# Optimization experiments

Hardware: AMD Instinct MI355X
Metric: run time of the kernel (lower is better)

## Reference

```python
import jax, jax.numpy as jnp
import numpy as np

B, T, C = 2, 2048, 2048
N_HEAD, N_GROUPS, HEAD_SIZE = 16, 4, 128
Q_PER_KV = N_HEAD // N_GROUPS


def setup_inputs() -> dict:
    key = jax.random.key(0)
    k1, k2, k3 = jax.random.split(key, 3)
    x = jax.random.normal(k1, (B, T, C), dtype=jnp.float32)
    # real RoPE cache: theta_i = 10000^{-2i/d}, cos/sin of shape [T, head_size//2]
    half = HEAD_SIZE // 2
    inv_freq = 1.0 / (10000.0 ** (jnp.arange(0, half, dtype=jnp.float32) / half))
    t = jnp.arange(T, dtype=jnp.float32)
    freqs = t[:, None] * inv_freq[None, :]  # [T, half]
    cos, sin = jnp.cos(freqs), jnp.sin(freqs)
    w_attn = jax.random.normal(k2, (C, (N_HEAD + 2 * N_GROUPS) * HEAD_SIZE), dtype=jnp.float32) * (C ** -0.5)
    w_proj = jax.random.normal(k3, (C, C), dtype=jnp.float32) * (C ** -0.5)
    return {"x": x, "cos": cos, "sin": sin, "w_attn": w_attn, "w_proj": w_proj}


def _apply_rope(x, cos, sin):
    # flash-attn style, interleaved=False: rotate first/second half of rotary dims
    # x: [B, T, H, D], cos/sin: [T, D//2]
    d2 = cos.shape[-1]
    x1, x2 = x[..., :d2], x[..., d2:2 * d2]
    c = cos[None, :, None, :]
    s = sin[None, :, None, :]
    return jnp.concatenate([x1 * c - x2 * s, x1 * s + x2 * c], axis=-1)


def reference(x, cos, sin, w_attn, w_proj):
    Bx, Tx, Cx = x.shape
    qkv = x @ w_attn  # [B, T, (n_head + 2*G)*hs]
    qkv = qkv.reshape(Bx, Tx, N_GROUPS, Q_PER_KV + 2, HEAD_SIZE)
    q = qkv[:, :, :, :Q_PER_KV, :].reshape(Bx, Tx, N_HEAD, HEAD_SIZE)
    k = qkv[:, :, :, Q_PER_KV, :]        # [B, T, G, hs]
    v = qkv[:, :, :, Q_PER_KV + 1, :]    # [B, T, G, hs]
    q = _apply_rope(q, cos, sin)
    k = _apply_rope(k, cos, sin)
    # GQA attention without materializing repeated K/V
    qg = q.reshape(Bx, Tx, N_GROUPS, Q_PER_KV, HEAD_SIZE)
    scale = 1.0 / jnp.sqrt(jnp.float32(HEAD_SIZE))
    scores = jnp.einsum('bqgpd,bkgd->bgpqk', qg, k) * scale  # [B,G,p,T,T]
    attn = jax.nn.softmax(scores, axis=-1)
    y = jnp.einsum('bgpqk,bkgd->bqgpd', attn, v)  # [B,T,G,p,hs]
    y = y.reshape(Bx, Tx, Cx)
    return y @ w_proj
```

## Files before the change

kernel.cpp:

```cpp
#include <hip/hip_runtime.h>
#include <stdint.h>

#define B_ 2
#define T_ 2048
#define C_ 2048
#define NH 16
#define NG 4
#define HS 128

typedef unsigned short u16;
typedef __bf16 bf16_t;
typedef bf16_t bf16x8 __attribute__((ext_vector_type(8)));
typedef float f32x4 __attribute__((ext_vector_type(4)));

__device__ __forceinline__ u16 f2bf(float f) {
    union { float f; uint32_t u; } v; v.f = f;
    uint32_t r = (v.u + 0x7fffu + ((v.u >> 16) & 1u)) >> 16;
    return (u16)r;
}
__device__ __forceinline__ float fast_ex2(float x) {
    float r; asm("v_exp_f32 %0, %1" : "=v"(r) : "v"(x)); return r;
}

__device__ __forceinline__ void transpose_body(const float* __restrict__ W, u16* __restrict__ Wt,
                                               int K, int N, int bx, int by, float (*tile)[33]) {
    int n0 = bx * 32, k0 = by * 32;
    int tx = threadIdx.x & 31, ty = threadIdx.x >> 5;
#pragma unroll
    for (int i = 0; i < 4; i++) {
        int r = ty + i * 8;
        tile[r][tx] = W[(size_t)(k0 + r) * N + (n0 + tx)];
    }
    __syncthreads();
#pragma unroll
    for (int i = 0; i < 4; i++) {
        int r = ty + i * 8;
        Wt[(size_t)(n0 + r) * K + (k0 + tx)] = f2bf(tile[tx][r]);
    }
}

__global__ void k_prep(const float* __restrict__ x, u16* __restrict__ xb,
                       const float* __restrict__ wa, u16* __restrict__ wat,
                       const float* __restrict__ wp, u16* __restrict__ wpt) {
    __shared__ float tile[32][33];
    int bid = blockIdx.x;
    if (bid < 8192) {
        int i = bid * 256 + threadIdx.x;
        float4 f = ((const float4*)x)[i];
        ushort4 o;
        o.x = f2bf(f.x); o.y = f2bf(f.y); o.z = f2bf(f.z); o.w = f2bf(f.w);
        ((ushort4*)xb)[i] = o;
    } else if (bid < 8192 + 6144) {
        int id = bid - 8192;
        transpose_body(wa, wat, 2048, 3072, id % 96, id / 96, tile);
    } else {
        int id = bid - 14336;
        transpose_body(wp, wpt, 2048, 2048, id % 64, id / 64, tile);
    }
}

#define MIDB { __builtin_amdgcn_s_barrier();                              \
               asm volatile("s_waitcnt lgkmcnt(0)" ::: "memory");         \
               __builtin_amdgcn_sched_barrier(0); }
#define ENDB { __builtin_amdgcn_s_barrier(); }
#define VMW4 { asm volatile("s_waitcnt vmcnt(4)" ::: "memory"); }
#define VMW0 { asm volatile("s_waitcnt vmcnt(0)" ::: "memory"); }

__device__ __forceinline__ void stage_half(const u16* __restrict__ g, int r0, int k0,
                                           u16* l, int tid) {
#pragma unroll
    for (int i = 0; i < 2; i++) {
        int c = tid + i * 512;
        int row = c >> 3, sl = c & 7;
        const u16* ga = g + (size_t)(r0 + row) * 2048 + k0 + (sl ^ (row & 7)) * 8;
        __builtin_amdgcn_global_load_lds((const __attribute__((address_space(1))) void*)ga,
                                         (__attribute__((address_space(3))) void*)(l + c * 8),
                                         16, 0, 0);
    }
}

__device__ __forceinline__ void stage_half64(const u16* __restrict__ g, int r0, int k0,
                                             u16* l, int tid) {
    int row = tid >> 3, sl = tid & 7;
    const u16* ga = g + (size_t)(r0 + row) * 2048 + k0 + (sl ^ (row & 7)) * 8;
    __builtin_amdgcn_global_load_lds((const __attribute__((address_space(1))) void*)ga,
                                     (__attribute__((address_space(3))) void*)(l + tid * 8),
                                     16, 0, 0);
}

__device__ __forceinline__ void rd_a(const u16* slot, int mq, int l16, int quad,
                                     bf16x8 (&af)[4][2]) {
#pragma unroll
    for (int mf = 0; mf < 4; mf++) {
        int row = mq * 64 + mf * 16 + l16;
#pragma unroll
        for (int kk = 0; kk < 2; kk++)
            af[mf][kk] = *(const bf16x8*)(slot + row * 64 + ((kk * 4 + quad) ^ (l16 & 7)) * 8);
    }
}

__device__ __forceinline__ void rd_b(const u16* slot, int nq, int sub, int l16, int quad,
                                     bf16x8 (&bs)[2][2]) {
#pragma unroll
    for (int g = 0; g < 2; g++) {
        int row = sub * 64 + (nq * 2 + g) * 16 + l16;
#pragma unroll
        for (int kk = 0; kk < 2; kk++)
            bs[g][kk] = *(const bf16x8*)(slot + row * 64 + ((kk * 4 + quad) ^ (l16 & 7)) * 8);
    }
}

template <int MQ, int NQ>
__device__ __forceinline__ void mm8(f32x4 (&acc)[8][4], const bf16x8 (&af)[4][2],
                                    const bf16x8 (&bs)[2][2]) {
    __builtin_amdgcn_s_setprio(1);
#pragma unroll
    for (int mf = 0; mf < 4; mf++)
#pragma unroll
        for (int g = 0; g < 2; g++)
#pragma unroll
            for (int kk = 0; kk < 2; kk++)
                acc[MQ * 4 + mf][NQ * 2 + g] = __builtin_amdgcn_mfma_f32_16x16x32_bf16(
                    af[mf][kk], bs[g][kk], acc[MQ * 4 + mf][NQ * 2 + g], 0, 0, 0);
    __builtin_amdgcn_s_setprio(0);
}

template <int MQ, int NQ>
__device__ __forceinline__ void mm4(f32x4 (&acc)[4][4], const bf16x8 (&af)[2][2],
                                    const bf16x8 (&bs)[2][2]) {
    __builtin_amdgcn_s_setprio(1);
#pragma unroll
    for (int mf = 0; mf < 2; mf++)
#pragma unroll
        for (int g = 0; g < 2; g++)
#pragma unroll
            for (int kk = 0; kk < 2; kk++)
                acc[MQ * 2 + mf][NQ * 2 + g] = __builtin_amdgcn_mfma_f32_16x16x32_bf16(
                    af[mf][kk], bs[g][kk], acc[MQ * 2 + mf][NQ * 2 + g], 0, 0, 0);
    __builtin_amdgcn_s_setprio(0);
}

__global__ __launch_bounds__(512, 2) void k_gemm_qkv(const u16* __restrict__ A,
                                                     const u16* __restrict__ Bt,
                                                     const float* __restrict__ cosb,
                                                     const float* __restrict__ sinb,
                                                     u16* __restrict__ qa,
                                                     u16* __restrict__ ka,
                                                     u16* __restrict__ vt) {
    extern __shared__ __align__(16) u16 sm[];
    const int tid = threadIdx.x;
    const int wave = tid >> 6, lane = tid & 63;
    const int quad = lane >> 4, l16 = lane & 15;
    const int wr = wave >> 2, wc = wave & 3;
    const int m0 = blockIdx.y * 256;
    const int brow = blockIdx.x * 256;

    const u16* As0 = sm + (0 * 2 + wr) * 8192;
    const u16* As1 = sm + (1 * 2 + wr) * 8192;
    const u16* Bs0 = sm + 32768 + (0 * 2 + (wc >> 1)) * 8192;
    const u16* Bs1 = sm + 32768 + (1 * 2 + (wc >> 1)) * 8192;

    f32x4 acc[8][4] = {};
    bf16x8 af[4][2], b0[2][2], b1[2][2];

    stage_half(A,  m0,        0,  sm + 0 * 8192, tid);
    stage_half(A,  m0 + 128,  0,  sm + 1 * 8192, tid);
    stage_half(Bt, brow,       0,  sm + 32768 + 0 * 8192, tid);
    stage_half(Bt, brow + 128, 0,  sm + 32768 + 1 * 8192, tid);
    stage_half(Bt, brow,       64, sm + 32768 + 2 * 8192, tid);
    stage_half(Bt, brow + 128, 64, sm + 32768 + 3 * 8192, tid);
    VMW4;
    __builtin_amdgcn_s_barrier();

    for (int i = 0; i < 15; i++) {
        const int k0 = i * 128;
        rd_a(As0, 0, l16, quad, af); rd_b(Bs0, 0, wc & 1, l16, quad, b0);
        stage_half(A, m0, k0 + 64, sm + 2 * 8192, tid);
        MIDB; mm8<0, 0>(acc, af, b0); ENDB;
        rd_b(Bs0, 1, wc & 1, l16, quad, b1);
        stage_half(A, m0 + 128, k0 + 64, sm + 3 * 8192, tid);
        MIDB; mm8<0, 1>(acc, af, b1); ENDB;
        rd_a(As0, 1, l16, quad, af);
        stage_half(Bt, brow, k0 + 128, sm + 32768 + 0 * 8192, tid);
        MIDB; mm8<1, 1>(acc, af, b1); ENDB;
        stage_half(Bt, brow + 128, k0 + 128, sm + 32768 + 1 * 8192, tid);
        MIDB; mm8<1, 0>(acc, af, b0); VMW4; ENDB;
        rd_a(As1, 0, l16, quad, af); rd_b(Bs1, 0, wc & 1, l16, quad, b0);
        stage_half(A, m0, k0 + 128, sm + 0 * 8192, tid);
        MIDB; mm8<0, 0>(acc, af, b0); ENDB;
        rd_b(Bs1, 1, wc & 1, l16, quad, b1);
        stage_half(A, m0 + 128, k0 + 128, sm + 1 * 8192, tid);
        MIDB; mm8<0, 1>(acc, af, b1); ENDB;
        rd_a(As1, 1, l16, quad, af);
        stage_half(Bt, brow, k0 + 192, sm + 32768 + 2 * 8192, tid);
        MIDB; mm8<1, 1>(acc, af, b1); ENDB;
        stage_half(Bt, brow + 128, k0 + 192, sm + 32768 + 3 * 8192, tid);
        MIDB; mm8<1, 0>(acc, af, b0); VMW4; ENDB;
    }
    {
        rd_a(As0, 0, l16, quad, af); rd_b(Bs0, 0, wc & 1, l16, quad, b0);
        stage_half(A, m0, 1984, sm + 2 * 8192, tid);
        MIDB; mm8<0, 0>(acc, af, b0); ENDB;
        rd_b(Bs0, 1, wc & 1, l16, quad, b1);
        stage_half(A, m0 + 128, 1984, sm + 3 * 8192, tid);
        MIDB; mm8<0, 1>(acc, af, b1); ENDB;
        rd_a(As0, 1, l16, quad, af);
        MIDB; mm8<1, 1>(acc, af, b1); ENDB;
        MIDB; mm8<1, 0>(acc, af, b0); VMW0; ENDB;
        rd_a(As1, 0, l16, quad, af); rd_b(Bs1, 0, wc & 1, l16, quad, b0);
        MIDB; mm8<0, 0>(acc, af, b0); ENDB;
        rd_b(Bs1, 1, wc & 1, l16, quad, b1);
        MIDB; mm8<0, 1>(acc, af, b1); ENDB;
        rd_a(As1, 1, l16, quad, af);
        MIDB; mm8<1, 1>(acc, af, b1); ENDB;
        MIDB; mm8<1, 0>(acc, af, b0); ENDB;
    }

    __syncthreads();
    const int s = blockIdx.x * 2 + (wc >> 1);
    const int stype = s % 6, grp = s / 6;
    const int dhalf = wc & 1;
    const int b = blockIdx.y >> 3;
    const int tb = (blockIdx.y & 7) * 256 + wr * 128;
    const int rid = wr * 2 + (wc >> 1);
    float4* xch = (float4*)sm;

    if (stype < 5 && dhalf == 1) {
#pragma unroll
        for (int mf = 0; mf < 8; mf++)
#pragma unroll
            for (int g = 0; g < 4; g++)
                xch[((rid * 8 + mf) * 4 + g) * 64 + quad * 16 + l16] = *(float4*)&acc[mf][g];
    }
    __syncthreads();
    if (stype < 5) {
        if (dhalf == 0) {
            const float QS = 0.08838834764831845f * 1.44269504088896341f;
            const float sc = (stype < 4) ? QS : 1.0f;
            u16* dst = (stype < 4) ? qa + ((size_t)(b * NH + grp * 4 + stype)) * T_ * 128
                                   : ka + ((size_t)(b * NG + grp)) * T_ * 128;
#pragma unroll
            for (int mf = 0; mf < 8; mf++)
#pragma unroll
                for (int g = 0; g < 4; g++) {
                    float4 x2 = xch[((rid * 8 + mf) * 4 + g) * 64 + quad * 16 + l16];
                    const float* x2p = (const float*)&x2;
                    int d = g * 16 + l16;
#pragma unroll
                    for (int r = 0; r < 4; r++) {
                        int t = tb + mf * 16 + quad * 4 + r;
                        float cc = cosb[t * 64 + d], ss = sinb[t * 64 + d];
                        float x1 = acc[mf][g][r];
                        u16* drow = dst + (size_t)t * 128;
                        drow[d] = f2bf((x1 * cc - x2p[r] * ss) * sc);
                        drow[d + 64] = f2bf((x1 * ss + x2p[r] * cc) * sc);
                    }
                }
        }
    } else {
        size_t vb = ((size_t)(b * NG + grp)) * 128;
#pragma unroll
        for (int mf = 0; mf < 8; mf++)
#pragma unroll
            for (int g = 0; g < 4; g++) {
                int d = dhalf * 64 + g * 16 + l16;
                int t0 = tb + mf * 16 + quad * 4;
                ushort4 o = make_ushort4(f2bf(acc[mf][g][0]), f2bf(acc[mf][g][1]),
                                         f2bf(acc[mf][g][2]), f2bf(acc[mf][g][3]));
                *(ushort4*)(vt + (vb + d) * T_ + t0) = o;
            }
    }
}

__global__ __launch_bounds__(512, 2) void k_gemm_bt(const u16* __restrict__ A,
                                                    const u16* __restrict__ Bt,
                                                    float* __restrict__ C) {
    extern __shared__ __align__(16) u16 sm[];
    const int tid = threadIdx.x;
    const int wave = tid >> 6, lane = tid & 63;
    const int quad = lane >> 4, l16 = lane & 15;
    const int wr = wave >> 2, wc = wave & 3;
    const int bh = wc >> 1, sub = wc & 1;
    const int m0 = blockIdx.y * 128, n0 = blockIdx.x * 256;

    const u16* As0 = sm + (0 * 2 + wr) * 4096;
    const u16* As1 = sm + (1 * 2 + wr) * 4096;
    const u16* Bs0 = sm + 16384 + (0 * 2 + bh) * 8192;
    const u16* Bs1 = sm + 16384 + (1 * 2 + bh) * 8192;

    f32x4 acc[4][4] = {};
    bf16x8 af[2][2], b0[2][2], b1[2][2];

    stage_half64(A, m0,       0, sm + 0 * 4096, tid);
    stage_half64(A, m0 + 64,  0, sm + 1 * 4096, tid);
    stage_half(Bt, n0,        0, sm + 16384 + 0 * 8192, tid);
    stage_half(Bt, n0 + 128,  0, sm + 16384 + 1 * 8192, tid);
    stage_half(Bt, n0,       64, sm + 16384 + 2 * 8192, tid);
    stage_half(Bt, n0 + 128, 64, sm + 16384 + 3 * 8192, tid);
    VMW4;
    __builtin_amdgcn_s_barrier();

    for (int i = 0; i < 15; i++) {
        const int k0 = i * 128;
        rd_b(As0, 0, 0, l16, quad, af); rd_b(Bs0, 0, sub, l16, quad, b0);
        stage_half64(A, m0, k0 + 64, sm + 2 * 4096, tid);
        MIDB; mm4<0, 0>(acc, af, b0); ENDB;
        rd_b(Bs0, 1, sub, l16, quad, b1);
        stage_half64(A, m0 + 64, k0 + 64, sm + 3 * 4096, tid);
        MIDB; mm4<0, 1>(acc, af, b1); ENDB;
        rd_b(As0, 1, 0, l16, quad, af);
        stage_half(Bt, n0, k0 + 128, sm + 16384 + 0 * 8192, tid);
        MIDB; mm4<1, 1>(acc, af, b1); ENDB;
        stage_half(Bt, n0 + 128, k0 + 128, sm + 16384 + 1 * 8192, tid);
        MIDB; mm4<1, 0>(acc, af, b0); VMW4; ENDB;
        rd_b(As1, 0, 0, l16, quad, af); rd_b(Bs1, 0, sub, l16, quad, b0);
        stage_half64(A, m0, k0 + 128, sm + 0 * 4096, tid);
        MIDB; mm4<0, 0>(acc, af, b0); ENDB;
        rd_b(Bs1, 1, sub, l16, quad, b1);
        stage_half64(A, m0 + 64, k0 + 128, sm + 1 * 4096, tid);
        MIDB; mm4<0, 1>(acc, af, b1); ENDB;
        rd_b(As1, 1, 0, l16, quad, af);
        stage_half(Bt, n0, k0 + 192, sm + 16384 + 2 * 8192, tid);
        MIDB; mm4<1, 1>(acc, af, b1); ENDB;
        stage_half(Bt, n0 + 128, k0 + 192, sm + 16384 + 3 * 8192, tid);
        MIDB; mm4<1, 0>(acc, af, b0); VMW4; ENDB;
    }
    {
        rd_b(As0, 0, 0, l16, quad, af); rd_b(Bs0, 0, sub, l16, quad, b0);
        stage_half64(A, m0, 1984, sm + 2 * 4096, tid);
        MIDB; mm4<0, 0>(acc, af, b0); ENDB;
        rd_b(Bs0, 1, sub, l16, quad, b1);
        stage_half64(A, m0 + 64, 1984, sm + 3 * 4096, tid);
        MIDB; mm4<0, 1>(acc, af, b1); ENDB;
        rd_b(As0, 1, 0, l16, quad, af);
        MIDB; mm4<1, 1>(acc, af, b1); ENDB;
        MIDB; mm4<1, 0>(acc, af, b0); VMW0; ENDB;
        rd_b(As1, 0, 0, l16, quad, af); rd_b(Bs1, 0, sub, l16, quad, b0);
        MIDB; mm4<0, 0>(acc, af, b0); ENDB;
        rd_b(Bs1, 1, sub, l16, quad, b1);
        MIDB; mm4<0, 1>(acc, af, b1); ENDB;
        rd_b(As1, 1, 0, l16, quad, af);
        MIDB; mm4<1, 1>(acc, af, b1); ENDB;
        MIDB; mm4<1, 0>(acc, af, b0); ENDB;
    }

#pragma unroll
    for (int am = 0; am < 4; am++)
#pragma unroll
        for (int an = 0; an < 4; an++)
#pragma unroll
            for (int r = 0; r < 4; r++) {
                int row = m0 + wr * 64 + am * 16 + quad * 4 + r;
                int col = n0 + wc * 64 + an * 16 + l16;
                C[(size_t)row * C_ + col] = acc[am][an][r];
            }
}

__global__ __launch_bounds__(256, 2) void k_attn(const u16* __restrict__ qa,
                                                 const u16* __restrict__ ka,
                                                 const u16* __restrict__ vt,
                                                 u16* __restrict__ ya) {
    __shared__ __align__(16) u16 smem[32768];
    const int tid = threadIdx.x;
    const int wave = tid >> 6, lane = tid & 63;
    const int quad = lane >> 4, l16 = lane & 15;
    const int qt = blockIdx.x, h = blockIdx.y, b = blockIdx.z;
    const int g = h >> 2;

    bf16x8 qf[2][4];
    {
        const u16* qbase = qa + (((size_t)(b * NH + h)) * T_ + qt * 128 + wave * 32 + l16) * 128;
#pragma unroll
        for (int t16 = 0; t16 < 2; t16++)
#pragma unroll
            for (int ks = 0; ks < 4; ks++)
                qf[t16][ks] = *(const bf16x8*)(qbase + t16 * 16 * 128 + ks * 32 + quad * 8);
    }
    const u16* kbase = ka + ((size_t)(b * NG + g)) * T_ * 128;
    const u16* vbase = vt + ((size_t)(b * NG + g)) * 128 * T_;

    int kdst[4], ksrc[4], vsrc[4], vdA[4], vdB[4];
#pragma unroll
    for (int i = 0; i < 4; i++) {
        int c = tid + i * 256;
        int row = c >> 4, seg = c & 15;
        kdst[i] = c * 8;
        ksrc[i] = row * 128 + (seg ^ (row & 15)) * 8;
        int d = c >> 3, m = c & 7;
        vsrc[i] = d * T_ + m * 8;
        int segA = (m >> 2) * 4 + (m & 1) * 2;
        int a4 = ((m >> 1) & 1) * 4;
        vdA[i] = d * 64 + (segA ^ (d & 7)) * 8 + a4;
        vdB[i] = d * 64 + ((segA + 1) ^ (d & 7)) * 8 + a4;
    }

    f32x4 yacc[2][8] = {};
    float lsum[2] = {0.f, 0.f};
    uint4 vr[4];

#pragma unroll
    for (int i = 0; i < 4; i++)
        __builtin_amdgcn_global_load_lds((const __attribute__((address_space(1))) void*)(kbase + ksrc[i]),
                                         (__attribute__((address_space(3))) void*)(smem + kdst[i]),
                                         16, 0, 0);
#pragma unroll
    for (int i = 0; i < 4; i++)
        vr[i] = *(const uint4*)(vbase + vsrc[i]);

    for (int kt = 0; kt < T_ / 64; kt++) {
        const int cur = kt & 1;
        u16* Kc = smem + cur * 8192;
        u16* Vc = smem + 16384 + cur * 8192;

        asm volatile("s_waitcnt vmcnt(0)" ::: "memory");
#pragma unroll
        for (int i = 0; i < 4; i++) {
            *(uint2*)&Vc[vdA[i]] = make_uint2(vr[i].x, vr[i].y);
            *(uint2*)&Vc[vdB[i]] = make_uint2(vr[i].z, vr[i].w);
        }
        __syncthreads();

        if (kt + 1 < T_ / 64) {
            u16* Kn = smem + (cur ^ 1) * 8192;
            const u16* kb = kbase + (size_t)(kt + 1) * 64 * 128;
#pragma unroll
            for (int i = 0; i < 4; i++)
                __builtin_amdgcn_global_load_lds((const __attribute__((address_space(1))) void*)(kb + ksrc[i]),
                                                 (__attribute__((address_space(3))) void*)(Kn + kdst[i]),
                                                 16, 0, 0);
            const u16* vb = vbase + (kt + 1) * 64;
#pragma unroll
            for (int i = 0; i < 4; i++)
                vr[i] = *(const uint4*)(vb + vsrc[i]);
        }

        f32x4 sacc[2][4] = {};
        __builtin_amdgcn_s_setprio(1);
#pragma unroll
        for (int ks = 0; ks < 4; ks++) {
#pragma unroll
            for (int ni = 0; ni < 4; ni++) {
                bf16x8 kf = *(const bf16x8*)&Kc[(ni * 16 + l16) * 128 + ((ks * 4 + quad) ^ l16) * 8];
                sacc[0][ni] = __builtin_amdgcn_mfma_f32_16x16x32_bf16(kf, qf[0][ks], sacc[0][ni], 0, 0, 0);
                sacc[1][ni] = __builtin_amdgcn_mfma_f32_16x16x32_bf16(kf, qf[1][ks], sacc[1][ni], 0, 0, 0);
            }
        }
        __builtin_amdgcn_s_setprio(0);

        uint32_t pk[2][4][2];
#pragma unroll
        for (int t16 = 0; t16 < 2; t16++) {
#pragma unroll
            for (int ni = 0; ni < 4; ni++) {
                float p0 = fast_ex2(sacc[t16][ni][0]);
                float p1 = fast_ex2(sacc[t16][ni][1]);
                float p2 = fast_ex2(sacc[t16][ni][2]);
                float p3 = fast_ex2(sacc[t16][ni][3]);
                lsum[t16] += (p0 + p1) + (p2 + p3);
                asm("v_cvt_pk_bf16_f32 %0, %1, %2" : "=v"(pk[t16][ni][0]) : "v"(p0), "v"(p1));
                asm("v_cvt_pk_bf16_f32 %0, %1, %2" : "=v"(pk[t16][ni][1]) : "v"(p2), "v"(p3));
            }
        }

        __builtin_amdgcn_s_setprio(1);
#pragma unroll
        for (int ks2 = 0; ks2 < 2; ks2++) {
            union { uint32_t u[4]; bf16x8 v; } pf0, pf1;
            pf0.u[0] = pk[0][2 * ks2][0];     pf0.u[1] = pk[0][2 * ks2][1];
            pf0.u[2] = pk[0][2 * ks2 + 1][0]; pf0.u[3] = pk[0][2 * ks2 + 1][1];
            pf1.u[0] = pk[1][2 * ks2][0];     pf1.u[1] = pk[1][2 * ks2][1];
            pf1.u[2] = pk[1][2 * ks2 + 1][0]; pf1.u[3] = pk[1][2 * ks2 + 1][1];
#pragma unroll
            for (int tile = 0; tile < 8; tile++) {
                bf16x8 vf = *(const bf16x8*)&Vc[(tile * 16 + l16) * 64 +
                                                ((ks2 * 4 + quad) ^ (l16 & 7)) * 8];
                yacc[0][tile] = __builtin_amdgcn_mfma_f32_16x16x32_bf16(vf, pf0.v, yacc[0][tile], 0, 0, 0);
                yacc[1][tile] = __builtin_amdgcn_mfma_f32_16x16x32_bf16(vf, pf1.v, yacc[1][tile], 0, 0, 0);
            }
        }
        __builtin_amdgcn_s_setprio(0);
    }

#pragma unroll
    for (int t16 = 0; t16 < 2; t16++) {
        lsum[t16] += __shfl_xor(lsum[t16], 16);
        lsum[t16] += __shfl_xor(lsum[t16], 32);
    }

    __syncthreads();
#pragma unroll
    for (int t16 = 0; t16 < 2; t16++) {
        float inv = 1.f / lsum[t16];
        int qrow = wave * 32 + t16 * 16 + l16;
#pragma unroll
        for (int tile = 0; tile < 8; tile++) {
#pragma unroll
            for (int cp = 0; cp < 2; cp++) {
                int d = tile * 16 + quad * 4 + cp * 2;
                uint32_t pv = (uint32_t)f2bf(yacc[t16][tile][cp * 2] * inv) |
                              ((uint32_t)f2bf(yacc[t16][tile][cp * 2 + 1] * inv) << 16);
                *(uint32_t*)&smem[qrow * 128 + ((d >> 3) ^ l16) * 8 + (d & 7)] = pv;
            }
        }
    }
    __syncthreads();
#pragma unroll
    for (int i = 0; i < 8; i++) {
        int cc = tid + i * 256;
        int row = cc >> 4, seg = cc & 15;
        uint4 dv = *(const uint4*)&smem[row * 128 + (seg ^ (row & 15)) * 8];
        size_t q = (size_t)(b * T_ + qt * 128 + row);
        *(uint4*)(ya + q * C_ + h * 128 + seg * 8) = dv;
    }
}

extern "C" void kernel_launch(void* const* d_in, const int* in_sizes, int n_in,
                              void* d_out, int out_size, void* d_ws, size_t ws_size,
                              hipStream_t stream) {
    (void)in_sizes; (void)n_in; (void)out_size; (void)ws_size;
    const float* x = (const float*)d_in[0];
    const float* cosb = (const float*)d_in[1];
    const float* sinb = (const float*)d_in[2];
    const float* w_attn = (const float*)d_in[3];
    const float* w_proj = (const float*)d_in[4];
    float* out = (float*)d_out;

    char* ws = (char*)d_ws;
    size_t off = 0;
    auto alloc = [&](size_t bytes) -> char* {
        char* p = ws + off;
        off += (bytes + 255) & ~(size_t)255;
        return p;
    };
    u16* xb  = (u16*)alloc((size_t)4096 * 2048 * 2);
    u16* wat = (u16*)alloc((size_t)3072 * 2048 * 2);
    u16* wpt = (u16*)alloc((size_t)2048 * 2048 * 2);
    u16* qa  = (u16*)alloc((size_t)B_ * NH * T_ * HS * 2);
    u16* ka  = (u16*)alloc((size_t)B_ * NG * T_ * HS * 2);
    u16* vt  = (u16*)alloc((size_t)B_ * NG * T_ * HS * 2);
    u16* ya  = xb;

    static bool smset = false;
    if (!smset) {
        (void)hipFuncSetAttribute((const void*)k_gemm_qkv,
                                  hipFuncAttributeMaxDynamicSharedMemorySize, 131072);
        (void)hipFuncSetAttribute((const void*)k_gemm_bt,
                                  hipFuncAttributeMaxDynamicSharedMemorySize, 98304);
        smset = true;
    }

    k_prep<<<dim3(18432), dim3(256), 0, stream>>>(x, xb, w_attn, wat, w_proj, wpt);
    k_gemm_qkv<<<dim3(12, 16), dim3(512), 131072, stream>>>(xb, wat, cosb, sinb, qa, ka, vt);
    k_attn<<<dim3(16, 16, 2), dim3(256), 0, stream>>>(qa, ka, vt, ya);
    k_gemm_bt<<<dim3(8, 32), dim3(512), 98304, stream>>>(ya, wpt, out);
}
```

Measured before the change: 280.9 us.

## Software-pipeline attention QK/softmax/PV across tiles and swizzle GEMM block order

The attention kernel is restructured so that the QK and softmax of tile kt overlap with the PV of tile kt-1. It uses two register sets for packed probabilities and a triple-buffered V tile in dynamic LDS (80KB). Both GEMM kernels also remap the linear block index with a stride-8 swizzle, so that blocks running at the same time share A/B panels in L2 or across XCDs. The larger LDS footprint may limit occupancy of the attention kernel to fewer blocks per CU.

```diff
diff --git a/kernel.cpp b/kernel.cpp
--- a/kernel.cpp
+++ b/kernel.cpp
@@ -152,8 +152,11 @@
     const int wave = tid >> 6, lane = tid & 63;
     const int quad = lane >> 4, l16 = lane & 15;
     const int wr = wave >> 2, wc = wave & 3;
-    const int m0 = blockIdx.y * 256;
-    const int brow = blockIdx.x * 256;
+    const int lin = blockIdx.x + 12 * blockIdx.y;
+    const int swz = (lin & 7) * 24 + (lin >> 3);
+    const int bx = swz % 12, by = swz / 12;
+    const int m0 = by * 256;
+    const int brow = bx * 256;
 
     const u16* As0 = sm + (0 * 2 + wr) * 8192;
     const u16* As1 = sm + (1 * 2 + wr) * 8192;
@@ -217,11 +220,11 @@
     }
 
     __syncthreads();
-    const int s = blockIdx.x * 2 + (wc >> 1);
+    const int s = bx * 2 + (wc >> 1);
     const int stype = s % 6, grp = s / 6;
     const int dhalf = wc & 1;
-    const int b = blockIdx.y >> 3;
-    const int tb = (blockIdx.y & 7) * 256 + wr * 128;
+    const int b = by >> 3;
+    const int tb = (by & 7) * 256 + wr * 128;
     const int rid = wr * 2 + (wc >> 1);
     float4* xch = (float4*)sm;
 
@@ -281,7 +284,10 @@
     const int quad = lane >> 4, l16 = lane & 15;
     const int wr = wave >> 2, wc = wave & 3;
     const int bh = wc >> 1, sub = wc & 1;
-    const int m0 = blockIdx.y * 128, n0 = blockIdx.x * 256;
+    const int lin = blockIdx.x + 8 * blockIdx.y;
+    const int swz = (lin & 7) * 32 + (lin >> 3);
+    const int bx = swz & 7, by = swz >> 3;
+    const int m0 = by * 128, n0 = bx * 256;
 
     const u16* As0 = sm + (0 * 2 + wr) * 4096;
     const u16* As1 = sm + (1 * 2 + wr) * 4096;
@@ -360,7 +366,9 @@
                                                  const u16* __restrict__ ka,
                                                  const u16* __restrict__ vt,
                                                  u16* __restrict__ ya) {
-    __shared__ __align__(16) u16 smem[32768];
+    extern __shared__ __align__(16) u16 smem[];
+    u16* Ks = smem;
+    u16* Vs = smem + 16384;
     const int tid = threadIdx.x;
     const int wave = tid >> 6, lane = tid & 63;
     const int quad = lane >> 4, l16 = lane & 15;
@@ -397,44 +405,37 @@
     f32x4 yacc[2][8] = {};
     float lsum[2] = {0.f, 0.f};
     uint4 vr[4];
-
-#pragma unroll
-    for (int i = 0; i < 4; i++)
-        __builtin_amdgcn_global_load_lds((const __attribute__((address_space(1))) void*)(kbase + ksrc[i]),
-                                         (__attribute__((address_space(3))) void*)(smem + kdst[i]),
-                                         16, 0, 0);
-#pragma unroll
-    for (int i = 0; i < 4; i++)
-        vr[i] = *(const uint4*)(vbase + vsrc[i]);
-
-    for (int kt = 0; kt < T_ / 64; kt++) {
-        const int cur = kt & 1;
-        u16* Kc = smem + cur * 8192;
-        u16* Vc = smem + 16384 + cur * 8192;
-
-        asm volatile("s_waitcnt vmcnt(0)" ::: "memory");
+    uint32_t pkA[2][4][2], pkB[2][4][2];
+    f32x4 sacc[2][4];
+
+    auto ISSUE_K = [&](int kt) {
+        u16* Kn = Ks + (kt & 1) * 8192;
+        const u16* kb = kbase + (size_t)kt * 8192;
+#pragma unroll
+        for (int i = 0; i < 4; i++)
+            __builtin_amdgcn_global_load_lds(
+                (const __attribute__((address_space(1))) void*)(kb + ksrc[i]),
+                (__attribute__((address_space(3))) void*)(Kn + kdst[i]), 16, 0, 0);
+    };
+    auto LOAD_V = [&](int kt) {
+        const u16* vb = vbase + kt * 64;
+#pragma unroll
+        for (int i = 0; i < 4; i++) vr[i] = *(const uint4*)(vb + vsrc[i]);
+    };
+    auto WRITE_V = [&](int kt) {
+        u16* Vc = Vs + (kt % 3) * 8192;
 #pragma unroll
         for (int i = 0; i < 4; i++) {
             *(uint2*)&Vc[vdA[i]] = make_uint2(vr[i].x, vr[i].y);
             *(uint2*)&Vc[vdB[i]] = make_uint2(vr[i].z, vr[i].w);
         }
-        __syncthreads();
-
-        if (kt + 1 < T_ / 64) {
-            u16* Kn = smem + (cur ^ 1) * 8192;
-            const u16* kb = kbase + (size_t)(kt + 1) * 64 * 128;
-#pragma unroll
-            for (int i = 0; i < 4; i++)
-                __builtin_amdgcn_global_load_lds((const __attribute__((address_space(1))) void*)(kb + ksrc[i]),
-                                                 (__attribute__((address_space(3))) void*)(Kn + kdst[i]),
-                                                 16, 0, 0);
-            const u16* vb = vbase + (kt + 1) * 64;
-#pragma unroll
-            for (int i = 0; i < 4; i++)
-                vr[i] = *(const uint4*)(vb + vsrc[i]);
-        }
-
-        f32x4 sacc[2][4] = {};
+    };
+    auto QK = [&](int kt) {
+        const u16* Kc = Ks + (kt & 1) * 8192;
+#pragma unroll
+        for (int t16 = 0; t16 < 2; t16++)
+#pragma unroll
+            for (int ni = 0; ni < 4; ni++) sacc[t16][ni] = f32x4{0.f, 0.f, 0.f, 0.f};
         __builtin_amdgcn_s_setprio(1);
 #pragma unroll
         for (int ks = 0; ks < 4; ks++) {
@@ -446,8 +447,8 @@
             }
         }
         __builtin_amdgcn_s_setprio(0);
-
-        uint32_t pk[2][4][2];
+    };
+    auto SM = [&](uint32_t (&pk)[2][4][2]) {
 #pragma unroll
         for (int t16 = 0; t16 < 2; t16++) {
 #pragma unroll
@@ -461,7 +462,9 @@
                 asm("v_cvt_pk_bf16_f32 %0, %1, %2" : "=v"(pk[t16][ni][1]) : "v"(p2), "v"(p3));
             }
         }
-
+    };
+    auto PV = [&](int kt, uint32_t (&pk)[2][4][2]) {
+        const u16* Vc = Vs + (kt % 3) * 8192;
         __builtin_amdgcn_s_setprio(1);
 #pragma unroll
         for (int ks2 = 0; ks2 < 2; ks2++) {
@@ -479,7 +482,23 @@
             }
         }
         __builtin_amdgcn_s_setprio(0);
-    }
+    };
+
+    ISSUE_K(0); LOAD_V(0);
+    VMW0; WRITE_V(0); __syncthreads();
+    ISSUE_K(1); LOAD_V(1);
+    QK(0); SM(pkA);
+    VMW0; WRITE_V(1); __syncthreads();
+    for (int kt = 1; kt <= 29; kt += 2) {
+        ISSUE_K(kt + 1); LOAD_V(kt + 1);
+        QK(kt); SM(pkB); PV(kt - 1, pkA);
+        VMW0; WRITE_V(kt + 1); __syncthreads();
+        ISSUE_K(kt + 2); LOAD_V(kt + 2);
+        QK(kt + 1); SM(pkA); PV(kt, pkB);
+        VMW0; WRITE_V(kt + 2); __syncthreads();
+    }
+    QK(31); SM(pkB); PV(30, pkA);
+    PV(31, pkB);
 
 #pragma unroll
     for (int t16 = 0; t16 < 2; t16++) {
@@ -546,11 +565,13 @@
                                   hipFuncAttributeMaxDynamicSharedMemorySize, 131072);
         (void)hipFuncSetAttribute((const void*)k_gemm_bt,
                                   hipFuncAttributeMaxDynamicSharedMemorySize, 98304);
+        (void)hipFuncSetAttribute((const void*)k_attn,
+                                  hipFuncAttributeMaxDynamicSharedMemorySize, 81920);
         smset = true;
     }
 
     k_prep<<<dim3(18432), dim3(256), 0, stream>>>(x, xb, w_attn, wat, w_proj, wpt);
     k_gemm_qkv<<<dim3(12, 16), dim3(512), 131072, stream>>>(xb, wat, cosb, sinb, qa, ka, vt);
-    k_attn<<<dim3(16, 16, 2), dim3(256), 0, stream>>>(qa, ka, vt, ya);
+    k_attn<<<dim3(16, 16, 2), dim3(256), 81920, stream>>>(qa, ka, vt, ya);
     k_gemm_bt<<<dim3(8, 32), dim3(512), 98304, stream>>>(ya, wpt, out);
 }
```

After: 306.6 us. 9.2% more time.
